# Optimization experiments

Hardware: AMD Instinct MI355X
Metric: run time of the kernel (lower is better)

The kernel has to match this reference:

```python
import jax, jax.numpy as jnp
import numpy as np

B, N, FEAT, H, HID = 2, 2048, 128, 5, 3
D = H * HID  # 15
NEG_INF = -9e15


def _gat(x, adj, W, a, concat):
    # x: [B,N,Fin], W: [Fin,Fout], a: [2*Fout]
    Wh = jnp.einsum('bnf,fo->bno', x, W)
    Fo = W.shape[1]
    f1 = Wh @ a[:Fo]          # [B,N]
    f2 = Wh @ a[Fo:]          # [B,N]
    e = jax.nn.leaky_relu(f1[:, :, None] + f2[:, None, :], 0.2)  # [B,N,N]
    att = jax.nn.softmax(jnp.where(adj > 0, e, NEG_INF), axis=-1)
    h = jnp.einsum('bij,bjo->bio', att, Wh)
    return (jax.nn.elu(h) if concat else h), att


def _diff_pool(x, adj, s):
    # torch_geometric.dense_diff_pool
    s = jax.nn.softmax(s, axis=-1)                       # [B,N,K]
    out = jnp.einsum('bnk,bnf->bkf', s, x)               # [B,K,F]
    out_adj = jnp.einsum('bnk,bnm,bml->bkl', s, adj, s)  # [B,K,K]
    link = jnp.linalg.norm(adj - jnp.einsum('bnk,bmk->bnm', s, s)) / adj.size
    ent = jnp.mean(jnp.sum(-s * jnp.log(s + 1e-15), axis=-1))
    return out, out_adj, link, ent


def setup_inputs() -> dict:
    key = jax.random.key(0)
    ks = jax.random.split(key, 16)
    p = lambda k, shp: (jax.random.normal(k, shp, jnp.float32) * 0.1)
    d = {}
    d['x'] = jax.random.normal(ks[0], (B, N, FEAT), jnp.float32)
    d['adj'] = jax.random.bernoulli(ks[1], 0.05, (B, N, N)).astype(jnp.float32)
    d['W_heads'] = p(ks[2], (H, FEAT, HID))
    d['a_heads'] = p(ks[3], (H, 2 * HID))
    d['W_out'] = p(ks[4], (D, D)); d['a_out'] = p(ks[5], (2 * D,))
    d['W_p1'] = p(ks[6], (D, 32)); d['a_p1'] = p(ks[7], (64,))
    d['lin1_w'] = p(ks[8], (32, 32)); d['lin1_b'] = p(ks[9], (32,))
    d['W_p2'] = p(ks[10], (D, 4)); d['a_p2'] = p(ks[11], (8,))
    d['lin2_w'] = p(ks[12], (4, 4)); d['lin2_b'] = p(ks[13], (4,))
    d['lin_w'] = p(ks[14], (4 * D, 2)); d['lin_b'] = p(ks[15], (2,))
    return d


def reference(x, adj, W_heads, a_heads, W_out, a_out, W_p1, a_p1,
              lin1_w, lin1_b, W_p2, a_p2, lin2_w, lin2_b, lin_w, lin_b):
    # eval mode: dropout = identity
    hs, atts = jax.vmap(lambda W, a: _gat(x, adj, W, a, True))(W_heads, a_heads)
    # hs: [H,B,N,HID] -> concat heads -> [B,N,H*HID]
    h = jnp.moveaxis(hs, 0, 2).reshape(x.shape[0], x.shape[1], -1)
    h = jax.nn.elu(_gat(h, adj, W_out, a_out, False)[0])
    # pool 1: N -> 32 clusters
    s1 = _gat(h, adj, W_p1, a_p1, True)[0] @ lin1_w + lin1_b
    h, adj2, link1, ent1 = _diff_pool(h, adj, s1)
    # pool 2: 32 -> 4 clusters
    s2 = _gat(h, adj2, W_p2, a_p2, True)[0] @ lin2_w + lin2_b
    h, adj3, link2, ent2 = _diff_pool(h, adj2, s2)
    ypred = h.reshape(h.shape[0], -1) @ lin_w + lin_b  # [B, class_num]
    loss = link1 + link2
    return ypred, loss, atts
```

## Files before the change

### kernel.cpp

```cpp
#include <hip/hip_runtime.h>
#include <hip/hip_bf16.h>

#define NN 2048
#define BB 2
#define RB 4096
#define CAP 192

__device__ __forceinline__ float lrelu(float v) { return v > 0.f ? v : 0.2f * v; }
__device__ __forceinline__ float eluf(float v) { return v > 0.f ? v : __expf(v) - 1.f; }

__device__ __forceinline__ float wredsum(float v) {
    for (int o = 32; o; o >>= 1) v += __shfl_down(v, o, 64);
    return v;
}
__device__ __forceinline__ float bsum(float v) {
    for (int m = 32; m; m >>= 1) v += __shfl_xor(v, m, 64);
    return v;
}
__device__ __forceinline__ float bmax(float v) {
    for (int m = 32; m; m >>= 1) v = fmaxf(v, __shfl_xor(v, m, 64));
    return v;
}

__global__ void k_zero(float* S) { if (threadIdx.x < 2) S[threadIdx.x] = 0.f; }

__global__ __launch_bounds__(256) void k_prep1(const float* __restrict__ x,
                                               const float* __restrict__ W,
                                               const float* __restrict__ a,
                                               float* __restrict__ Wh1,
                                               float* __restrict__ f1o,
                                               float* __restrict__ f2o) {
    const int tid = threadIdx.x, w = tid >> 6, lane = tid & 63;
    const int r = blockIdx.x * 4 + w;
    const float xa = x[(size_t)r * 128 + lane];
    const float xb = x[(size_t)r * 128 + 64 + lane];
#pragma unroll
    for (int h = 0; h < 5; ++h) {
        float f1v = 0.f, f2v = 0.f;
#pragma unroll
        for (int f = 0; f < 3; ++f) {
            const float w0 = W[h * 384 + lane * 3 + f];
            const float w1 = W[h * 384 + (lane + 64) * 3 + f];
            const float d = bsum(xa * w0 + xb * w1);
            if (lane == 0) Wh1[((size_t)h * RB + r) * 3 + f] = d;
            f1v += d * a[h * 6 + f];
            f2v += d * a[h * 6 + 3 + f];
        }
        if (lane == 0) { f1o[h * RB + r] = f1v; f2o[h * RB + r] = f2v; }
    }
}

__global__ __launch_bounds__(320) void k_gata(const float* __restrict__ adj,
                                              const float* __restrict__ Wh,
                                              const float* __restrict__ f1,
                                              const float* __restrict__ f2,
                                              const float* __restrict__ W_out,
                                              const float* __restrict__ a_out,
                                              float* __restrict__ Wh2,
                                              float* __restrict__ f1_2,
                                              float* __restrict__ f2_2,
                                              float* __restrict__ sinv,
                                              int* __restrict__ nnzcnt,
                                              unsigned short* __restrict__ nnzidx,
                                              float* __restrict__ S) {
    __shared__ unsigned short nidx[CAP];
    __shared__ float h1row[15];
    __shared__ int ncnt;
    const int tid = threadIdx.x, h = tid >> 6, lane = tid & 63;
    const int r = blockIdx.x;
    const int b = r >> 11, i = r & (NN - 1);
    const float* arow = adj + ((size_t)b * NN + i) * NN;

    if (tid == 0) ncnt = 0;
    __syncthreads();
    for (int j = tid; j < NN; j += 320) {
        if (arow[j] > 0.f) {
            const int pos = atomicAdd(&ncnt, 1);
            if (pos < CAP) nidx[pos] = (unsigned short)j;
        }
    }
    __syncthreads();
    const int cnt = min(ncnt, CAP);
    if (tid == 0) { nnzcnt[r] = cnt; atomicAdd(S, (float)ncnt); }
    for (int p = tid; p < cnt; p += 320) nnzidx[(size_t)r * CAP + p] = nidx[p];

    const float f1i = f1[h * RB + r];
    const float* f2h = f2 + h * RB + b * NN;
    const float* WhB = Wh + ((size_t)h * RB + b * NN) * 3;
    float lsum = 0.f, h0 = 0.f, h1v = 0.f, h2v = 0.f;
    for (int q = lane; q < cnt; q += 64) {
        const int j = nidx[q];
        const float p = __expf(lrelu(f1i + f2h[j]));
        lsum += p;
        const float* wv = WhB + (size_t)j * 3;
        h0 += p * wv[0]; h1v += p * wv[1]; h2v += p * wv[2];
    }
    const float inv = 1.f / bsum(lsum);
    h0 = bsum(h0); h1v = bsum(h1v); h2v = bsum(h2v);
    if (lane == 0) {
        sinv[h * RB + r] = inv;
        h1row[h * 3 + 0] = eluf(h0 * inv);
        h1row[h * 3 + 1] = eluf(h1v * inv);
        h1row[h * 3 + 2] = eluf(h2v * inv);
    }
    __syncthreads();
    if (h == 0) {
        float whv = 0.f;
        if (lane < 15) {
#pragma unroll
            for (int f = 0; f < 15; f++) whv += h1row[f] * W_out[f * 15 + lane];
            Wh2[(size_t)r * 15 + lane] = whv;
        }
        float s1p = (lane < 15) ? whv * a_out[lane] : 0.f;
        float s2p = (lane < 15) ? whv * a_out[15 + lane] : 0.f;
        s1p = wredsum(s1p); s2p = wredsum(s2p);
        if (lane == 0) { f1_2[r] = s1p; f2_2[r] = s2p; }
    }
}

__global__ __launch_bounds__(256) void k_scatter(const float* __restrict__ f1,
                                                 const float* __restrict__ f2,
                                                 const float* __restrict__ sinv,
                                                 const int* __restrict__ nnzcnt,
                                                 const unsigned short* __restrict__ nnzidx,
                                                 float* __restrict__ att_out) {
    const int idx = blockIdx.x;
    const int h = idx >> 12;
    const int r = idx & (RB - 1);
    const int b = r >> 11, i = r & (NN - 1);
    const int tid = threadIdx.x;
    float* ao = att_out + (((size_t)h * BB + b) * NN + i) * NN;
    if (tid < 3) ao[tid] = 0.f;
    if (tid == 3) ao[2047] = 0.f;
    float4* ao4 = (float4*)(ao + 3);
    for (int v = tid; v < 511; v += 256) ao4[v] = make_float4(0.f, 0.f, 0.f, 0.f);
    __syncthreads();
    const int cnt = nnzcnt[r];
    const float f1i = f1[h * RB + r];
    const float* f2h = f2 + h * RB + b * NN;
    const float inv = sinv[h * RB + r];
    for (int q = tid; q < cnt; q += 256) {
        const int j = nnzidx[(size_t)r * CAP + q];
        ao[j] = __expf(lrelu(f1i + f2h[j])) * inv;
    }
}

__global__ __launch_bounds__(256) void k_gat2(const int* __restrict__ nnzcnt,
                                              const unsigned short* __restrict__ nnzidx,
                                              const float* __restrict__ Wh2,
                                              const float* __restrict__ f1_2,
                                              const float* __restrict__ f2_2,
                                              const float* __restrict__ W_p1,
                                              const float* __restrict__ a_p1,
                                              float* __restrict__ h2,
                                              float* __restrict__ Wh3,
                                              float* __restrict__ f1_3,
                                              float* __restrict__ f2_3) {
    __shared__ unsigned short sidx[4][CAP];
    __shared__ float sp[4][CAP];
    __shared__ float h2l[4][15];
    const int tid = threadIdx.x, w = tid >> 6, lane = tid & 63;
    const int r = blockIdx.x * 4 + w;
    const int b = r >> 11;
    const int cnt = nnzcnt[r];
    for (int q = lane; q < cnt; q += 64) sidx[w][q] = nnzidx[(size_t)r * CAP + q];
    __syncthreads();

    const float f1i = f1_2[r];
    float ee[3];
    float lm = -3.0e38f;
#pragma unroll
    for (int t3 = 0; t3 < 3; ++t3) {
        const int q = lane + 64 * t3;
        if (q < cnt) {
            const int j = sidx[w][q];
            const float v = lrelu(f1i + f2_2[b * NN + j]);
            ee[t3] = v;
            lm = fmaxf(lm, v);
        } else ee[t3] = -3.0e38f;
    }
    const float m = bmax(lm);
    float lsum = 0.f;
#pragma unroll
    for (int t3 = 0; t3 < 3; ++t3) {
        const int q = lane + 64 * t3;
        if (q < cnt) {
            const float p = __expf(ee[t3] - m);
            sp[w][q] = p;
            lsum += p;
        }
    }
    const float inv = 1.f / bsum(lsum);
    __syncthreads();

    const int g4 = lane / 15, f = lane - g4 * 15;
    float acc = 0.f;
    if (lane < 60) {
        for (int q = g4; q < cnt; q += 4)
            acc += sp[w][q] * Wh2[(size_t)(b * NN + sidx[w][q]) * 15 + f];
    }
    acc += __shfl_down(acc, 15, 64);
    acc += __shfl_down(acc, 30, 64);
    if (lane < 15) {
        const float v = eluf(acc * inv);
        h2[(size_t)r * 15 + f] = v;
        h2l[w][f] = v;
    }
    __syncthreads();

    float wh3 = 0.f;
    if (lane < 32) {
#pragma unroll
        for (int ff = 0; ff < 15; ++ff) wh3 += h2l[w][ff] * W_p1[ff * 32 + lane];
        Wh3[(size_t)r * 32 + lane] = wh3;
    }
    float s1p = (lane < 32) ? wh3 * a_p1[lane] : 0.f;
    float s2p = (lane < 32) ? wh3 * a_p1[32 + lane] : 0.f;
    s1p = bsum(s1p); s2p = bsum(s2p);
    if (lane == 0) { f1_3[r] = s1p; f2_3[r] = s2p; }
}

__global__ __launch_bounds__(256) void k_gat3(const int* __restrict__ nnzcnt,
                                              const unsigned short* __restrict__ nnzidx,
                                              const float* __restrict__ Wh3,
                                              const float* __restrict__ f1_3,
                                              const float* __restrict__ f2_3,
                                              const float* __restrict__ lw,
                                              const float* __restrict__ lb,
                                              float* __restrict__ s_out) {
    __shared__ unsigned short sidx[4][CAP];
    __shared__ float sp[4][CAP];
    __shared__ float h3l[4][32];
    const int tid = threadIdx.x, w = tid >> 6, lane = tid & 63;
    const int r = blockIdx.x * 4 + w;
    const int b = r >> 11;
    const int cnt = nnzcnt[r];
    for (int q = lane; q < cnt; q += 64) sidx[w][q] = nnzidx[(size_t)r * CAP + q];
    __syncthreads();

    const float f1i = f1_3[r];
    float ee[3];
    float lm = -3.0e38f;
#pragma unroll
    for (int t3 = 0; t3 < 3; ++t3) {
        const int q = lane + 64 * t3;
        if (q < cnt) {
            const int j = sidx[w][q];
            const float v = lrelu(f1i + f2_3[b * NN + j]);
            ee[t3] = v;
            lm = fmaxf(lm, v);
        } else ee[t3] = -3.0e38f;
    }
    const float m = bmax(lm);
    float lsum = 0.f;
#pragma unroll
    for (int t3 = 0; t3 < 3; ++t3) {
        const int q = lane + 64 * t3;
        if (q < cnt) {
            const float p = __expf(ee[t3] - m);
            sp[w][q] = p;
            lsum += p;
        }
    }
    const float inv = 1.f / bsum(lsum);
    __syncthreads();

    const int g2 = lane >> 5, f = lane & 31;
    float acc = 0.f;
    for (int q = g2; q < cnt; q += 2)
        acc += sp[w][q] * Wh3[(size_t)(b * NN + sidx[w][q]) * 32 + f];
    acc += __shfl_xor(acc, 32, 64);
    if (lane < 32) h3l[w][f] = eluf(acc * inv);
    __syncthreads();

    float z = -3.0e38f;
    if (lane < 32) {
        z = lb[lane];
#pragma unroll
        for (int ff = 0; ff < 32; ++ff) z += h3l[w][ff] * lw[ff * 32 + lane];
    }
    const float zm = bmax(z);
    const float p2 = (lane < 32) ? __expf(z - zm) : 0.f;
    const float zinv = 1.f / bsum(p2);
    if (lane < 32) s_out[(size_t)r * 32 + lane] = p2 * zinv;
}

__global__ __launch_bounds__(256) void k_tsp(const int* __restrict__ nnzcnt,
                                             const unsigned short* __restrict__ nnzidx,
                                             const float* __restrict__ smat,
                                             float* __restrict__ t) {
    __shared__ unsigned short sidx[4][CAP];
    const int tid = threadIdx.x, w = tid >> 6, lane = tid & 63;
    const int r = blockIdx.x * 4 + w;
    const int b = r >> 11;
    const int cnt = nnzcnt[r];
    for (int q = lane; q < cnt; q += 64) sidx[w][q] = nnzidx[(size_t)r * CAP + q];
    __syncthreads();
    const int g2 = lane >> 5, f = lane & 31;
    float acc = 0.f;
    for (int q = g2; q < cnt; q += 2)
        acc += smat[(size_t)(b * NN + sidx[w][q]) * 32 + f];
    acc += __shfl_xor(acc, 32, 64);
    if (lane < 32) t[(size_t)r * 32 + f] = acc;
}

__global__ __launch_bounds__(256) void k_pstats(const float* __restrict__ s,
                                                const float* __restrict__ t,
                                                const float* __restrict__ h2,
                                                float* __restrict__ adj2,
                                                float* __restrict__ hp1,
                                                float* __restrict__ S) {
    const int bk = blockIdx.x;
    const int b = bk >> 5, k = bk & 31;
    const int tid = threadIdx.x, lane = tid & 63, wid = tid >> 6;
    __shared__ float redG[128], redT[128], redH[60];
    __shared__ float gsq[32], tval[32];
    float aG[32], aT[32], aH[15];
#pragma unroll
    for (int l = 0; l < 32; l++) { aG[l] = 0.f; aT[l] = 0.f; }
#pragma unroll
    for (int f = 0; f < 15; f++) aH[f] = 0.f;
    const float* sb = s + (size_t)b * NN * 32;
    const float* tb = t + (size_t)b * NN * 32;
    const float* hb = h2 + (size_t)b * NN * 15;
    for (int n = tid; n < NN; n += 256) {
        const float sv = sb[(size_t)n * 32 + k];
        const float* sj = sb + (size_t)n * 32;
        const float* tj = tb + (size_t)n * 32;
        const float* hj = hb + (size_t)n * 15;
#pragma unroll
        for (int l = 0; l < 32; l++) { aG[l] += sv * sj[l]; aT[l] += sv * tj[l]; }
#pragma unroll
        for (int f = 0; f < 15; f++) aH[f] += sv * hj[f];
    }
#pragma unroll
    for (int l = 0; l < 32; l++) {
        const float vG = wredsum(aG[l]);
        const float vT = wredsum(aT[l]);
        if (lane == 0) { redG[wid * 32 + l] = vG; redT[wid * 32 + l] = vT; }
    }
#pragma unroll
    for (int f = 0; f < 15; f++) {
        const float vH = wredsum(aH[f]);
        if (lane == 0) redH[wid * 15 + f] = vH;
    }
    __syncthreads();
    if (tid < 32) {
        const float G = redG[tid] + redG[32 + tid] + redG[64 + tid] + redG[96 + tid];
        const float T = redT[tid] + redT[32 + tid] + redT[64 + tid] + redT[96 + tid];
        adj2[((size_t)b * 32 + k) * 32 + tid] = T;
        gsq[tid] = G * G;
        tval[tid] = T;
    }
    if (tid < 15) hp1[((size_t)b * 32 + k) * 15 + tid] = redH[tid] + redH[15 + tid] + redH[30 + tid] + redH[45 + tid];
    __syncthreads();
    if (tid == 0) {
        float ss = 0.f;
#pragma unroll
        for (int l = 0; l < 32; l++) ss += gsq[l];
        atomicAdd(S, ss - 2.f * tval[k]);
    }
}

__global__ __launch_bounds__(64) void k_pool2(const float* __restrict__ hp1,
                                              const float* __restrict__ adj2,
                                              const float* __restrict__ Wp2, const float* __restrict__ a2,
                                              const float* __restrict__ l2w, const float* __restrict__ l2b,
                                              const float* __restrict__ lw, const float* __restrict__ lb,
                                              float* __restrict__ S2, float* __restrict__ out) {
    __shared__ float hp[480], a2l[1024], wh[128], f1l[32], f2l[32], s2l[128], hp2[60];
    const int b = blockIdx.x, tid = threadIdx.x;
    for (int idx = tid; idx < 480; idx += 64) hp[idx] = hp1[b * 480 + idx];
    for (int idx = tid; idx < 1024; idx += 64) a2l[idx] = adj2[b * 1024 + idx];
    __syncthreads();
    for (int idx = tid; idx < 128; idx += 64) {
        const int n = idx >> 2, c = idx & 3;
        float acc = 0.f;
#pragma unroll
        for (int f = 0; f < 15; f++) acc += hp[n * 15 + f] * Wp2[f * 4 + c];
        wh[idx] = acc;
    }
    __syncthreads();
    if (tid < 32) {
        float s1 = 0.f, s2 = 0.f;
#pragma unroll
        for (int c = 0; c < 4; c++) {
            s1 += wh[tid * 4 + c] * a2[c];
            s2 += wh[tid * 4 + c] * a2[4 + c];
        }
        f1l[tid] = s1;
        f2l[tid] = s2;
    }
    __syncthreads();
    if (tid < 32) {
        const int n = tid;
        float e[32];
        float m = -3.0e38f;
#pragma unroll
        for (int j = 0; j < 32; j++) {
            const float v = lrelu(f1l[n] + f2l[j]);
            e[j] = a2l[n * 32 + j] > 0.f ? v : -9.0e15f;
            m = fmaxf(m, e[j]);
        }
        float sum = 0.f;
#pragma unroll
        for (int j = 0; j < 32; j++) { e[j] = __expf(e[j] - m); sum += e[j]; }
        const float inv = 1.f / sum;
        float h4[4];
#pragma unroll
        for (int c = 0; c < 4; c++) {
            float acc = 0.f;
#pragma unroll
            for (int j = 0; j < 32; j++) acc += e[j] * wh[j * 4 + c];
            h4[c] = eluf(acc * inv);
        }
        float z[4];
        float zm = -3.0e38f;
#pragma unroll
        for (int c = 0; c < 4; c++) {
            float acc = l2b[c];
#pragma unroll
            for (int c2 = 0; c2 < 4; c2++) acc += h4[c2] * l2w[c2 * 4 + c];
            z[c] = acc;
            zm = fmaxf(zm, acc);
        }
        float zs = 0.f;
#pragma unroll
        for (int c = 0; c < 4; c++) { z[c] = __expf(z[c] - zm); zs += z[c]; }
        const float zi = 1.f / zs;
#pragma unroll
        for (int c = 0; c < 4; c++) s2l[n * 4 + c] = z[c] * zi;
    }
    __syncthreads();
    if (tid < 60) {
        const int c = tid / 15, f = tid % 15;
        float acc = 0.f;
#pragma unroll
        for (int n = 0; n < 32; n++) acc += s2l[n * 4 + c] * hp[n * 15 + f];
        hp2[tid] = acc;
    }
    float lacc = 0.f;
    for (int idx = tid; idx < 1024; idx += 64) {
        const int n = idx >> 5, mm = idx & 31;
        float d = 0.f;
#pragma unroll
        for (int c = 0; c < 4; c++) d += s2l[n * 4 + c] * s2l[mm * 4 + c];
        const float df = a2l[idx] - d;
        lacc += df * df;
    }
    lacc = wredsum(lacc);
    if (tid == 0) atomicAdd(S2, lacc);
    __syncthreads();
    if (tid < 2) {
        float acc = lb[tid];
#pragma unroll
        for (int k2 = 0; k2 < 60; k2++) acc += hp2[k2] * lw[k2 * 2 + tid];
        out[b * 2 + tid] = acc;
    }
}

__global__ void k_final(const float* __restrict__ S, float* __restrict__ out) {
    const float loss = sqrtf(S[0]) / 8388608.f + sqrtf(S[1]) / 2048.f;
    out[4] = loss;
}

extern "C" void kernel_launch(void* const* d_in, const int* in_sizes, int n_in,
                              void* d_out, int out_size, void* d_ws, size_t ws_size,
                              hipStream_t stream) {
    const float* x      = (const float*)d_in[0];
    const float* adj    = (const float*)d_in[1];
    const float* W_h    = (const float*)d_in[2];
    const float* a_h    = (const float*)d_in[3];
    const float* W_out  = (const float*)d_in[4];
    const float* a_out  = (const float*)d_in[5];
    const float* W_p1   = (const float*)d_in[6];
    const float* a_p1   = (const float*)d_in[7];
    const float* lin1_w = (const float*)d_in[8];
    const float* lin1_b = (const float*)d_in[9];
    const float* W_p2   = (const float*)d_in[10];
    const float* a_p2   = (const float*)d_in[11];
    const float* lin2_w = (const float*)d_in[12];
    const float* lin2_b = (const float*)d_in[13];
    const float* lin_w  = (const float*)d_in[14];
    const float* lin_b  = (const float*)d_in[15];
    float* outp = (float*)d_out;

    float* W = (float*)d_ws;
    float* Wh1  = W;
    float* f1_1 = Wh1 + 61440;
    float* f2_1 = f1_1 + 20480;
    float* Wh2  = f2_1 + 20480;
    float* f1_2 = Wh2 + 61440;
    float* f2_2 = f1_2 + 4096;
    float* h2   = f2_2 + 4096;
    float* Wh3  = h2 + 61440;
    float* f1_3 = Wh3 + 131072;
    float* f2_3 = f1_3 + 4096;
    float* s    = f2_3 + 4096;
    float* t    = s + 131072;
    float* hp1  = t + 131072;
    float* adj2 = hp1 + 960;
    float* S    = adj2 + 2048;
    float* sinv = S + 2;
    int* nnzcnt = (int*)(sinv + 20480);
    unsigned short* nnzidx = (unsigned short*)(nnzcnt + RB);

    k_zero<<<1, 64, 0, stream>>>(S);
    k_prep1<<<RB / 4, 256, 0, stream>>>(x, W_h, a_h, Wh1, f1_1, f2_1);
    k_gata<<<RB, 320, 0, stream>>>(adj, Wh1, f1_1, f2_1, W_out, a_out,
                                   Wh2, f1_2, f2_2, sinv, nnzcnt, nnzidx, S);
    k_scatter<<<5 * RB, 256, 0, stream>>>(f1_1, f2_1, sinv, nnzcnt, nnzidx, outp + 5);
    k_gat2<<<RB / 4, 256, 0, stream>>>(nnzcnt, nnzidx, Wh2, f1_2, f2_2,
                                       W_p1, a_p1, h2, Wh3, f1_3, f2_3);
    k_gat3<<<RB / 4, 256, 0, stream>>>(nnzcnt, nnzidx, Wh3, f1_3, f2_3,
                                       lin1_w, lin1_b, s);
    k_tsp<<<RB / 4, 256, 0, stream>>>(nnzcnt, nnzidx, s, t);
    k_pstats<<<64, 256, 0, stream>>>(s, t, h2, adj2, hp1, S);
    k_pool2<<<BB, 64, 0, stream>>>(hp1, adj2, W_p2, a_p2, lin2_w, lin2_b, lin_w, lin_b, S + 1, outp);
    k_final<<<1, 1, 0, stream>>>(S, outp);
}
```

Before: 209.7 us.

## Write attention output in one pass using adjacency bitmask; fold tiny kernels away

The adjacency bitmask per row is built in k_gata and stored globally. The attention-output kernel then writes every element once as a float4, computing the value or zero from the mask, instead of zero-filling and then scattering the nonzeros. The k_zero and k_final launches are folded into k_prep1 and a single-block k_pool2 that loops over the batch and computes the loss. The aim is to remove the double write to the 168MB attention tensor and two launches, at the cost of recomputing exp for masked lanes and serialising pool2 into one block.

```diff
diff --git a/kernel.cpp b/kernel.cpp
--- a/kernel.cpp
+++ b/kernel.cpp
@@ -21,15 +21,15 @@
     for (int m = 32; m; m >>= 1) v = fmaxf(v, __shfl_xor(v, m, 64));
     return v;
 }
-
-__global__ void k_zero(float* S) { if (threadIdx.x < 2) S[threadIdx.x] = 0.f; }
 
 __global__ __launch_bounds__(256) void k_prep1(const float* __restrict__ x,
                                                const float* __restrict__ W,
                                                const float* __restrict__ a,
                                                float* __restrict__ Wh1,
                                                float* __restrict__ f1o,
-                                               float* __restrict__ f2o) {
+                                               float* __restrict__ f2o,
+                                               float* __restrict__ S) {
+    if (blockIdx.x == 0 && threadIdx.x < 2) S[threadIdx.x] = 0.f;
     const int tid = threadIdx.x, w = tid >> 6, lane = tid & 63;
     const int r = blockIdx.x * 4 + w;
     const float xa = x[(size_t)r * 128 + lane];
@@ -62,8 +62,10 @@
                                               float* __restrict__ sinv,
                                               int* __restrict__ nnzcnt,
                                               unsigned short* __restrict__ nnzidx,
+                                              unsigned int* __restrict__ maskG,
                                               float* __restrict__ S) {
     __shared__ unsigned short nidx[CAP];
+    __shared__ unsigned int mask[64];
     __shared__ float h1row[15];
     __shared__ int ncnt;
     const int tid = threadIdx.x, h = tid >> 6, lane = tid & 63;
@@ -72,16 +74,19 @@
     const float* arow = adj + ((size_t)b * NN + i) * NN;
 
     if (tid == 0) ncnt = 0;
+    if (tid < 64) mask[tid] = 0u;
     __syncthreads();
     for (int j = tid; j < NN; j += 320) {
         if (arow[j] > 0.f) {
             const int pos = atomicAdd(&ncnt, 1);
             if (pos < CAP) nidx[pos] = (unsigned short)j;
+            atomicOr(&mask[j >> 5], 1u << (j & 31));
         }
     }
     __syncthreads();
     const int cnt = min(ncnt, CAP);
     if (tid == 0) { nnzcnt[r] = cnt; atomicAdd(S, (float)ncnt); }
+    if (tid < 64) maskG[r * 64 + tid] = mask[tid];
     for (int p = tid; p < cnt; p += 320) nnzidx[(size_t)r * CAP + p] = nidx[p];
 
     const float f1i = f1[h * RB + r];
@@ -118,30 +123,37 @@
     }
 }
 
-__global__ __launch_bounds__(256) void k_scatter(const float* __restrict__ f1,
-                                                 const float* __restrict__ f2,
-                                                 const float* __restrict__ sinv,
-                                                 const int* __restrict__ nnzcnt,
-                                                 const unsigned short* __restrict__ nnzidx,
-                                                 float* __restrict__ att_out) {
-    const int idx = blockIdx.x;
-    const int h = idx >> 12;
-    const int r = idx & (RB - 1);
-    const int b = r >> 11, i = r & (NN - 1);
-    const int tid = threadIdx.x;
-    float* ao = att_out + (((size_t)h * BB + b) * NN + i) * NN;
-    if (tid < 3) ao[tid] = 0.f;
-    if (tid == 3) ao[2047] = 0.f;
-    float4* ao4 = (float4*)(ao + 3);
-    for (int v = tid; v < 511; v += 256) ao4[v] = make_float4(0.f, 0.f, 0.f, 0.f);
-    __syncthreads();
-    const int cnt = nnzcnt[r];
-    const float f1i = f1[h * RB + r];
-    const float* f2h = f2 + h * RB + b * NN;
-    const float inv = sinv[h * RB + r];
-    for (int q = tid; q < cnt; q += 256) {
-        const int j = nnzidx[(size_t)r * CAP + q];
-        ao[j] = __expf(lrelu(f1i + f2h[j])) * inv;
+__global__ __launch_bounds__(256) void k_wratts(const float* __restrict__ f1,
+                                                const float* __restrict__ f2,
+                                                const float* __restrict__ sinv,
+                                                const unsigned int* __restrict__ maskG,
+                                                float* __restrict__ att_out) {
+    const int total = 5 * RB * 512;
+    const int stride = gridDim.x * 256;
+    for (int g = blockIdx.x * 256 + threadIdx.x; g < total; g += stride) {
+        const int hr = g >> 9;
+        const int v  = g & 511;
+        const int r  = hr & (RB - 1);
+        const int hb = hr >> 11;
+        const float f1i = f1[hr];
+        const float inv = sinv[hr];
+        const float* f2h = f2 + (size_t)hb * NN;
+        const unsigned int* mrow = maskG + r * 64;
+        float* ao = att_out + (size_t)hr * NN;
+        if (v == 511) {
+#pragma unroll
+            for (int e = 0; e < 3; ++e)
+                ao[e] = ((mrow[0] >> e) & 1u) ? __expf(lrelu(f1i + f2h[e])) * inv : 0.f;
+            ao[2047] = ((mrow[63] >> 31) & 1u) ? __expf(lrelu(f1i + f2h[2047])) * inv : 0.f;
+        } else {
+            const int j0 = 3 + 4 * v;
+            float4 o;
+            o.x = ((mrow[(j0    ) >> 5] >> ((j0    ) & 31)) & 1u) ? __expf(lrelu(f1i + f2h[j0    ])) * inv : 0.f;
+            o.y = ((mrow[(j0 + 1) >> 5] >> ((j0 + 1) & 31)) & 1u) ? __expf(lrelu(f1i + f2h[j0 + 1])) * inv : 0.f;
+            o.z = ((mrow[(j0 + 2) >> 5] >> ((j0 + 2) & 31)) & 1u) ? __expf(lrelu(f1i + f2h[j0 + 2])) * inv : 0.f;
+            o.w = ((mrow[(j0 + 3) >> 5] >> ((j0 + 3) & 31)) & 1u) ? __expf(lrelu(f1i + f2h[j0 + 3])) * inv : 0.f;
+            ((float4*)(ao + 3))[v] = o;
+        }
     }
 }
 
@@ -367,101 +379,101 @@
                                               const float* __restrict__ Wp2, const float* __restrict__ a2,
                                               const float* __restrict__ l2w, const float* __restrict__ l2b,
                                               const float* __restrict__ lw, const float* __restrict__ lb,
-                                              float* __restrict__ S2, float* __restrict__ out) {
+                                              const float* __restrict__ S, float* __restrict__ out) {
     __shared__ float hp[480], a2l[1024], wh[128], f1l[32], f2l[32], s2l[128], hp2[60];
-    const int b = blockIdx.x, tid = threadIdx.x;
-    for (int idx = tid; idx < 480; idx += 64) hp[idx] = hp1[b * 480 + idx];
-    for (int idx = tid; idx < 1024; idx += 64) a2l[idx] = adj2[b * 1024 + idx];
-    __syncthreads();
-    for (int idx = tid; idx < 128; idx += 64) {
-        const int n = idx >> 2, c = idx & 3;
-        float acc = 0.f;
-#pragma unroll
-        for (int f = 0; f < 15; f++) acc += hp[n * 15 + f] * Wp2[f * 4 + c];
-        wh[idx] = acc;
-    }
-    __syncthreads();
-    if (tid < 32) {
-        float s1 = 0.f, s2 = 0.f;
-#pragma unroll
-        for (int c = 0; c < 4; c++) {
-            s1 += wh[tid * 4 + c] * a2[c];
-            s2 += wh[tid * 4 + c] * a2[4 + c];
-        }
-        f1l[tid] = s1;
-        f2l[tid] = s2;
-    }
-    __syncthreads();
-    if (tid < 32) {
-        const int n = tid;
-        float e[32];
-        float m = -3.0e38f;
-#pragma unroll
-        for (int j = 0; j < 32; j++) {
-            const float v = lrelu(f1l[n] + f2l[j]);
-            e[j] = a2l[n * 32 + j] > 0.f ? v : -9.0e15f;
-            m = fmaxf(m, e[j]);
-        }
-        float sum = 0.f;
-#pragma unroll
-        for (int j = 0; j < 32; j++) { e[j] = __expf(e[j] - m); sum += e[j]; }
-        const float inv = 1.f / sum;
-        float h4[4];
-#pragma unroll
-        for (int c = 0; c < 4; c++) {
+    const int tid = threadIdx.x;
+    float link2 = 0.f;
+    for (int b = 0; b < BB; ++b) {
+        __syncthreads();
+        for (int idx = tid; idx < 480; idx += 64) hp[idx] = hp1[b * 480 + idx];
+        for (int idx = tid; idx < 1024; idx += 64) a2l[idx] = adj2[b * 1024 + idx];
+        __syncthreads();
+        for (int idx = tid; idx < 128; idx += 64) {
+            const int n = idx >> 2, c = idx & 3;
             float acc = 0.f;
 #pragma unroll
-            for (int j = 0; j < 32; j++) acc += e[j] * wh[j * 4 + c];
-            h4[c] = eluf(acc * inv);
-        }
-        float z[4];
-        float zm = -3.0e38f;
-#pragma unroll
-        for (int c = 0; c < 4; c++) {
-            float acc = l2b[c];
-#pragma unroll
-            for (int c2 = 0; c2 < 4; c2++) acc += h4[c2] * l2w[c2 * 4 + c];
-            z[c] = acc;
-            zm = fmaxf(zm, acc);
-        }
-        float zs = 0.f;
-#pragma unroll
-        for (int c = 0; c < 4; c++) { z[c] = __expf(z[c] - zm); zs += z[c]; }
-        const float zi = 1.f / zs;
-#pragma unroll
-        for (int c = 0; c < 4; c++) s2l[n * 4 + c] = z[c] * zi;
-    }
-    __syncthreads();
-    if (tid < 60) {
-        const int c = tid / 15, f = tid % 15;
-        float acc = 0.f;
-#pragma unroll
-        for (int n = 0; n < 32; n++) acc += s2l[n * 4 + c] * hp[n * 15 + f];
-        hp2[tid] = acc;
-    }
-    float lacc = 0.f;
-    for (int idx = tid; idx < 1024; idx += 64) {
-        const int n = idx >> 5, mm = idx & 31;
-        float d = 0.f;
-#pragma unroll
-        for (int c = 0; c < 4; c++) d += s2l[n * 4 + c] * s2l[mm * 4 + c];
-        const float df = a2l[idx] - d;
-        lacc += df * df;
-    }
-    lacc = wredsum(lacc);
-    if (tid == 0) atomicAdd(S2, lacc);
-    __syncthreads();
-    if (tid < 2) {
-        float acc = lb[tid];
-#pragma unroll
-        for (int k2 = 0; k2 < 60; k2++) acc += hp2[k2] * lw[k2 * 2 + tid];
-        out[b * 2 + tid] = acc;
-    }
-}
-
-__global__ void k_final(const float* __restrict__ S, float* __restrict__ out) {
-    const float loss = sqrtf(S[0]) / 8388608.f + sqrtf(S[1]) / 2048.f;
-    out[4] = loss;
+            for (int f = 0; f < 15; f++) acc += hp[n * 15 + f] * Wp2[f * 4 + c];
+            wh[idx] = acc;
+        }
+        __syncthreads();
+        if (tid < 32) {
+            float s1 = 0.f, s2 = 0.f;
+#pragma unroll
+            for (int c = 0; c < 4; c++) {
+                s1 += wh[tid * 4 + c] * a2[c];
+                s2 += wh[tid * 4 + c] * a2[4 + c];
+            }
+            f1l[tid] = s1;
+            f2l[tid] = s2;
+        }
+        __syncthreads();
+        if (tid < 32) {
+            const int n = tid;
+            float e[32];
+            float m = -3.0e38f;
+#pragma unroll
+            for (int j = 0; j < 32; j++) {
+                const float v = lrelu(f1l[n] + f2l[j]);
+                e[j] = a2l[n * 32 + j] > 0.f ? v : -9.0e15f;
+                m = fmaxf(m, e[j]);
+            }
+            float sum = 0.f;
+#pragma unroll
+            for (int j = 0; j < 32; j++) { e[j] = __expf(e[j] - m); sum += e[j]; }
+            const float inv = 1.f / sum;
+            float h4[4];
+#pragma unroll
+            for (int c = 0; c < 4; c++) {
+                float acc = 0.f;
+#pragma unroll
+                for (int j = 0; j < 32; j++) acc += e[j] * wh[j * 4 + c];
+                h4[c] = eluf(acc * inv);
+            }
+            float z[4];
+            float zm = -3.0e38f;
+#pragma unroll
+            for (int c = 0; c < 4; c++) {
+                float acc = l2b[c];
+#pragma unroll
+                for (int c2 = 0; c2 < 4; c2++) acc += h4[c2] * l2w[c2 * 4 + c];
+                z[c] = acc;
+                zm = fmaxf(zm, acc);
+            }
+            float zs = 0.f;
+#pragma unroll
+            for (int c = 0; c < 4; c++) { z[c] = __expf(z[c] - zm); zs += z[c]; }
+            const float zi = 1.f / zs;
+#pragma unroll
+            for (int c = 0; c < 4; c++) s2l[n * 4 + c] = z[c] * zi;
+        }
+        __syncthreads();
+        if (tid < 60) {
+            const int c = tid / 15, f = tid % 15;
+            float acc = 0.f;
+#pragma unroll
+            for (int n = 0; n < 32; n++) acc += s2l[n * 4 + c] * hp[n * 15 + f];
+            hp2[tid] = acc;
+        }
+        float lacc = 0.f;
+        for (int idx = tid; idx < 1024; idx += 64) {
+            const int n = idx >> 5, mm = idx & 31;
+            float d = 0.f;
+#pragma unroll
+            for (int c = 0; c < 4; c++) d += s2l[n * 4 + c] * s2l[mm * 4 + c];
+            const float df = a2l[idx] - d;
+            lacc += df * df;
+        }
+        lacc = wredsum(lacc);
+        link2 += lacc;
+        __syncthreads();
+        if (tid < 2) {
+            float acc = lb[tid];
+#pragma unroll
+            for (int k2 = 0; k2 < 60; k2++) acc += hp2[k2] * lw[k2 * 2 + tid];
+            out[b * 2 + tid] = acc;
+        }
+    }
+    if (tid == 0) out[4] = sqrtf(S[0]) / 8388608.f + sqrtf(link2) / 2048.f;
 }
 
 extern "C" void kernel_launch(void* const* d_in, const int* in_sizes, int n_in,
@@ -504,18 +516,17 @@
     float* sinv = S + 2;
     int* nnzcnt = (int*)(sinv + 20480);
     unsigned short* nnzidx = (unsigned short*)(nnzcnt + RB);
-
-    k_zero<<<1, 64, 0, stream>>>(S);
-    k_prep1<<<RB / 4, 256, 0, stream>>>(x, W_h, a_h, Wh1, f1_1, f2_1);
+    unsigned int* maskG = (unsigned int*)(nnzidx + (size_t)RB * CAP);
+
+    k_prep1<<<RB / 4, 256, 0, stream>>>(x, W_h, a_h, Wh1, f1_1, f2_1, S);
     k_gata<<<RB, 320, 0, stream>>>(adj, Wh1, f1_1, f2_1, W_out, a_out,
-                                   Wh2, f1_2, f2_2, sinv, nnzcnt, nnzidx, S);
-    k_scatter<<<5 * RB, 256, 0, stream>>>(f1_1, f2_1, sinv, nnzcnt, nnzidx, outp + 5);
+                                   Wh2, f1_2, f2_2, sinv, nnzcnt, nnzidx, maskG, S);
+    k_wratts<<<4096, 256, 0, stream>>>(f1_1, f2_1, sinv, maskG, outp + 5);
     k_gat2<<<RB / 4, 256, 0, stream>>>(nnzcnt, nnzidx, Wh2, f1_2, f2_2,
                                        W_p1, a_p1, h2, Wh3, f1_3, f2_3);
     k_gat3<<<RB / 4, 256, 0, stream>>>(nnzcnt, nnzidx, Wh3, f1_3, f2_3,
                                        lin1_w, lin1_b, s);
     k_tsp<<<RB / 4, 256, 0, stream>>>(nnzcnt, nnzidx, s, t);
     k_pstats<<<64, 256, 0, stream>>>(s, t, h2, adj2, hp1, S);
-    k_pool2<<<BB, 64, 0, stream>>>(hp1, adj2, W_p2, a_p2, lin2_w, lin2_b, lin_w, lin_b, S + 1, outp);
-    k_final<<<1, 1, 0, stream>>>(S, outp);
-}
+    k_pool2<<<1, 64, 0, stream>>>(hp1, adj2, W_p2, a_p2, lin2_w, lin2_b, lin_w, lin_b, S, outp);
+}
```

Result: slower. 227.5 us (+8.5%).
